# Performance work log

Measured on AMD Instinct MI355X. Metric: run time of the kernel, lower is better.

## Reference

```python
import jax, jax.numpy as jnp
import numpy as np

D_MODEL = 1024
D_FF = 4096
N_HEADS = 16
D_HEAD = D_MODEL // N_HEADS
EPS = 1e-6


def setup_inputs() -> dict:
    key = jax.random.key(0)
    ks = jax.random.split(key, 12)
    B, S = 8, 1024
    s = 1.0 / np.sqrt(D_MODEL)
    inp = {
        "x": jax.random.normal(ks[0], (B, S, D_MODEL), dtype=jnp.float32),
        "mask": jnp.zeros((B, S, S), dtype=bool),
        "gamma1": jnp.ones((D_MODEL,), jnp.float32),
        "beta1": jnp.zeros((D_MODEL,), jnp.float32),
        "Wq": jax.random.normal(ks[1], (D_MODEL, D_MODEL), jnp.float32) * s,
        "bq": jnp.zeros((D_MODEL,), jnp.float32),
        "Wk": jax.random.normal(ks[2], (D_MODEL, D_MODEL), jnp.float32) * s,
        "bk": jnp.zeros((D_MODEL,), jnp.float32),
        "Wv": jax.random.normal(ks[3], (D_MODEL, D_MODEL), jnp.float32) * s,
        "bv": jnp.zeros((D_MODEL,), jnp.float32),
        "Wo": jax.random.normal(ks[4], (D_MODEL, D_MODEL), jnp.float32) * s,
        "bo": jnp.zeros((D_MODEL,), jnp.float32),
        "gamma2": jnp.ones((D_MODEL,), jnp.float32),
        "beta2": jnp.zeros((D_MODEL,), jnp.float32),
        "W1": jax.random.normal(ks[5], (D_MODEL, D_FF), jnp.float32) * s,
        "b1": jnp.zeros((D_FF,), jnp.float32),
        "W2": jax.random.normal(ks[6], (D_FF, D_MODEL), jnp.float32) * (1.0 / np.sqrt(D_FF)),
        "b2": jnp.zeros((D_MODEL,), jnp.float32),
    }
    return inp


def layer_norm(x, gamma, beta):
    mean = jnp.mean(x, axis=-1, keepdims=True)
    var = jnp.mean(jnp.square(x - mean), axis=-1, keepdims=True)  # unbiased=False
    return gamma * (x - mean) / jnp.sqrt(var + EPS) + beta


def mha(x, mask, Wq, bq, Wk, bk, Wv, bv, Wo, bo):
    B, S, _ = x.shape
    # projections: [B,S,D] -> [B,H,S,dh]
    q = (x @ Wq + bq).reshape(B, S, N_HEADS, D_HEAD).transpose(0, 2, 1, 3)
    k = (x @ Wk + bk).reshape(B, S, N_HEADS, D_HEAD).transpose(0, 2, 1, 3)
    v = (x @ Wv + bv).reshape(B, S, N_HEADS, D_HEAD).transpose(0, 2, 1, 3)
    # scores: [B,H,Sq,Sk]
    scores = jnp.einsum("bhqd,bhkd->bhqk", q, k) / np.sqrt(D_HEAD)
    scores = jnp.where(mask[:, None, :, :], -jnp.inf, scores)
    attn = jax.nn.softmax(scores, axis=-1)
    out = jnp.einsum("bhqk,bhkd->bhqd", attn, v)  # [B,H,Sq,dh]
    out = out.transpose(0, 2, 1, 3).reshape(B, S, D_MODEL)
    return out @ Wo + bo


def reference(x, mask, gamma1, beta1, Wq, bq, Wk, bk, Wv, bv, Wo, bo,
              gamma2, beta2, W1, b1, W2, b2):
    # pre-layer-norm variant per source: x = ln1(x); x = x + attn(x); x = ln2(x); x = x + ff(x)
    x = layer_norm(x, gamma1, beta1)
    x = x + mha(x, mask, Wq, bq, Wk, bk, Wv, bv, Wo, bo)
    x = layer_norm(x, gamma2, beta2)
    ff = jax.nn.relu(x @ W1 + b1) @ W2 + b2
    return x + ff
```

## Files before the change

### kernel.cpp

```cpp
#include <hip/hip_runtime.h>
#include <hip/hip_bf16.h>

typedef __bf16 bf16;
typedef __bf16 bf16x8 __attribute__((ext_vector_type(8)));
typedef __bf16 bf16x4 __attribute__((ext_vector_type(4)));
typedef float  f32x4  __attribute__((ext_vector_type(4)));

#define N_HEADS 16
#define D_HEAD  64
#define SEQ     1024
#define BATCH   8
#define MROWS   (BATCH * SEQ)

__device__ __forceinline__ void gld_lds16(const void* g, void* l) {
    __builtin_amdgcn_global_load_lds(
        (const __attribute__((address_space(1))) void*)g,
        (__attribute__((address_space(3))) void*)l, 16, 0, 0);
}

__global__ __launch_bounds__(256)
void wconv_t(const float* __restrict__ W, bf16* __restrict__ Wt, int K, int N)
{
    __shared__ float tile[32][33];
    const int tx = threadIdx.x & 31, ty = threadIdx.x >> 5;
    const int nb = blockIdx.x * 32, kb = blockIdx.y * 32;
    #pragma unroll
    for (int i = 0; i < 4; ++i)
        tile[ty + i * 8][tx] = W[(size_t)(kb + ty + i * 8) * N + nb + tx];
    __syncthreads();
    #pragma unroll
    for (int i = 0; i < 4; ++i)
        Wt[(size_t)(nb + ty + i * 8) * K + kb + tx] = (bf16)tile[tx][ty + i * 8];
}

__global__ __launch_bounds__(256)
void bconcat(const float* __restrict__ bq, const float* __restrict__ bk,
             const float* __restrict__ bv, float* __restrict__ o)
{
    const int i = blockIdx.x * 256 + threadIdx.x;
    if (i < 1024)       o[i] = bq[i];
    else if (i < 2048)  o[i] = bk[i - 1024];
    else if (i < 3072)  o[i] = bv[i - 2048];
}

__global__ __launch_bounds__(256)
void mask_pack(const unsigned char* __restrict__ m,
               unsigned long long* __restrict__ bits)
{
    const int i = blockIdx.x * 256 + threadIdx.x;
    unsigned long long b = __ballot(m[i] != 0);
    if ((threadIdx.x & 63) == 0) bits[i >> 6] = b;
}

__global__ __launch_bounds__(256)
void ln_kernel(const float* __restrict__ x, const float* __restrict__ g,
               const float* __restrict__ b, bf16* __restrict__ obf,
               float* __restrict__ of)
{
    const int row = blockIdx.x;
    const int tid = threadIdx.x;
    const float4 v = ((const float4*)(x + (size_t)row * 1024))[tid];
    float s  = v.x + v.y + v.z + v.w;
    float sq = v.x * v.x + v.y * v.y + v.z * v.z + v.w * v.w;
    #pragma unroll
    for (int off = 32; off; off >>= 1) {
        s  += __shfl_down(s, off);
        sq += __shfl_down(sq, off);
    }
    __shared__ float red[8];
    const int wid = tid >> 6, lid = tid & 63;
    if (lid == 0) { red[wid] = s; red[4 + wid] = sq; }
    __syncthreads();
    if (tid == 0) {
        float ts = red[0] + red[1] + red[2] + red[3];
        float tq = red[4] + red[5] + red[6] + red[7];
        float mean = ts * (1.f / 1024.f);
        float var  = tq * (1.f / 1024.f) - mean * mean;
        red[0] = mean;
        red[1] = rsqrtf(var + 1e-6f);
    }
    __syncthreads();
    const float mean = red[0], rstd = red[1];
    const float4 gg = ((const float4*)g)[tid];
    const float4 bb = ((const float4*)b)[tid];
    float y0 = (v.x - mean) * rstd * gg.x + bb.x;
    float y1 = (v.y - mean) * rstd * gg.y + bb.y;
    float y2 = (v.z - mean) * rstd * gg.z + bb.z;
    float y3 = (v.w - mean) * rstd * gg.w + bb.w;
    float4 o; o.x = y0; o.y = y1; o.z = y2; o.w = y3;
    ((float4*)(of + (size_t)row * 1024))[tid] = o;
    bf16x4 ob; ob[0] = (bf16)y0; ob[1] = (bf16)y1; ob[2] = (bf16)y2; ob[3] = (bf16)y3;
    ((bf16x4*)(obf + (size_t)row * 1024))[tid] = ob;
}

template <int EPI>
__global__ __launch_bounds__(256)
void gemm_bt(const bf16* __restrict__ A, const bf16* __restrict__ Bt,
             const float* __restrict__ bias, const float* __restrict__ resid,
             void* __restrict__ Cout, int M, int N, int K, int nbx)
{
    __shared__ __attribute__((aligned(16))) bf16 a_lds[128 * 64];
    __shared__ __attribute__((aligned(16))) bf16 b_lds[128 * 64];
    const int tid = threadIdx.x;
    const int l = tid & 63, w = tid >> 6;
    const int lo = l & 15, hi = l >> 4;

    const int nwg = gridDim.x;
    const int nid = (blockIdx.x & 7) * (nwg >> 3) + (blockIdx.x >> 3);
    const int bx = nid % nbx, by = nid / nbx;
    const int m0 = by * 128, n0 = bx * 128;

    const int wrow = (w >> 1) * 64, wcol = (w & 1) * 64;
    const int srow = tid >> 3;
    const int c8   = tid & 7;
    const int c8g  = c8 ^ (srow & 7);

    f32x4 acc[4][4];
    #pragma unroll
    for (int i = 0; i < 4; ++i)
        #pragma unroll
        for (int j = 0; j < 4; ++j) acc[i][j] = f32x4{0.f, 0.f, 0.f, 0.f};

    const int nkt = K >> 6;
    for (int kt = 0; kt < nkt; ++kt) {
        __syncthreads();
        const int kc = kt * 64 + c8g * 8;
        #pragma unroll
        for (int blk = 0; blk < 4; ++blk) {
            const int row = blk * 32 + srow;
            gld_lds16(A  + (size_t)(m0 + row) * K + kc, &a_lds[row * 64 + c8 * 8]);
            gld_lds16(Bt + (size_t)(n0 + row) * K + kc, &b_lds[row * 64 + c8 * 8]);
        }
        asm volatile("s_waitcnt vmcnt(0)" ::: "memory");
        __syncthreads();

        #pragma unroll
        for (int kk2 = 0; kk2 < 2; ++kk2) {
            bf16x8 af[4], bfr[4];
            #pragma unroll
            for (int m = 0; m < 4; ++m) {
                const int row = wrow + m * 16 + lo;
                const int ch = ((kk2 * 4 + hi) ^ (lo & 7)) << 3;
                af[m] = *(const bf16x8*)&a_lds[row * 64 + ch];
            }
            #pragma unroll
            for (int n = 0; n < 4; ++n) {
                const int row = wcol + n * 16 + lo;
                const int ch = ((kk2 * 4 + hi) ^ (lo & 7)) << 3;
                bfr[n] = *(const bf16x8*)&b_lds[row * 64 + ch];
            }
            #pragma unroll
            for (int m = 0; m < 4; ++m)
                #pragma unroll
                for (int n = 0; n < 4; ++n)
                    acc[m][n] = __builtin_amdgcn_mfma_f32_16x16x32_bf16(af[m], bfr[n], acc[m][n], 0, 0, 0);
        }
    }

    #pragma unroll
    for (int m = 0; m < 4; ++m) {
        const int Rbase = m0 + wrow + m * 16 + hi * 4;
        #pragma unroll
        for (int n = 0; n < 4; ++n) {
            const int Cc = n0 + wcol + n * 16 + lo;
            const float bv = bias[Cc];
            #pragma unroll
            for (int r = 0; r < 4; ++r) {
                const int Rr = Rbase + r;
                float vv = acc[m][n][r] + bv;
                if (EPI == 0) {
                    const int b_ = Rr >> 10, s_ = Rr & 1023;
                    const int which = Cc >> 10;
                    const int cc = Cc & 1023;
                    const int h_ = cc >> 6, d_ = cc & 63;
                    ((bf16*)Cout)[(size_t)which * ((size_t)MROWS * 1024) +
                                  (((size_t)(b_ * 16 + h_) * 1024 + s_) << 6) + d_] = (bf16)vv;
                } else if (EPI == 1) {
                    vv += resid[(size_t)Rr * N + Cc];
                    ((float*)Cout)[(size_t)Rr * N + Cc] = vv;
                } else {
                    vv = fmaxf(vv, 0.f);
                    ((bf16*)Cout)[(size_t)Rr * N + Cc] = (bf16)vv;
                }
            }
        }
    }
}

__global__ __launch_bounds__(256)
void attn_kernel(const bf16* __restrict__ q, const bf16* __restrict__ k,
                 const bf16* __restrict__ v,
                 const unsigned long long* __restrict__ mbits,
                 bf16* __restrict__ ctx)
{
    __shared__ __attribute__((aligned(16))) bf16 q_lds[64][72];
    __shared__ __attribute__((aligned(16))) bf16 k_lds[64][72];
    __shared__ __attribute__((aligned(16))) bf16 vt_lds[64][72];
    __shared__ __attribute__((aligned(16))) bf16 p_lds[4][16][72];

    const int id = blockIdx.x;
    const int swz = (id & 7) * 256 + (id >> 3);
    const int qt = swz & 15;
    const int bh = swz >> 4;
    const int hh = bh & 15, bb = bh >> 4;
    const int tid = threadIdx.x;
    const int w = tid >> 6, l = tid & 63;
    const int lo = l & 15, hi = l >> 4;

    {
        const bf16* qg = q + ((size_t)bh * SEQ + qt * 64) * D_HEAD;
        #pragma unroll
        for (int i = 0; i < 2; ++i) {
            const int e = (i * 256 + tid) * 8;
            const int r = e >> 6, c = e & 63;
            *(uint4*)&q_lds[r][c] = *(const uint4*)(qg + r * 64 + c);
        }
    }

    f32x4 oacc[4];
    float m_r[4], l_r[4];
    #pragma unroll
    for (int i = 0; i < 4; ++i) {
        oacc[i] = f32x4{0.f, 0.f, 0.f, 0.f};
        m_r[i] = -__builtin_inff();
        l_r[i] = 0.f;
    }

    for (int kt = 0; kt < 16; ++kt) {
        __syncthreads();
        const bf16* kg = k + ((size_t)bh * SEQ + kt * 64) * D_HEAD;
        const bf16* vg = v + ((size_t)bh * SEQ + kt * 64) * D_HEAD;
        #pragma unroll
        for (int i = 0; i < 2; ++i) {
            const int e = (i * 256 + tid) * 8;
            const int r = e >> 6, c = e & 63;
            *(uint4*)&k_lds[r][c] = *(const uint4*)(kg + r * 64 + c);
            uint4 tv = *(const uint4*)(vg + r * 64 + c);
            const bf16* pv = (const bf16*)&tv;
            const int colS = r ^ (((c >> 3) & 7) << 3);
            #pragma unroll
            for (int j = 0; j < 8; ++j) vt_lds[c + j][colS] = pv[j];
        }
        unsigned long long mb[4];
        #pragma unroll
        for (int r = 0; r < 4; ++r) {
            const int qrow = qt * 64 + w * 16 + hi * 4 + r;
            mb[r] = mbits[((((size_t)bb << 10) | qrow) << 4) + kt];
        }
        __syncthreads();

        f32x4 sf[4];
        #pragma unroll
        for (int ct = 0; ct < 4; ++ct) {
            f32x4 sa = f32x4{0.f, 0.f, 0.f, 0.f};
            #pragma unroll
            for (int kk = 0; kk < 2; ++kk) {
                bf16x8 a   = *(const bf16x8*)&q_lds[w * 16 + lo][kk * 32 + hi * 8];
                bf16x8 bfr = *(const bf16x8*)&k_lds[ct * 16 + lo][kk * 32 + hi * 8];
                sa = __builtin_amdgcn_mfma_f32_16x16x32_bf16(a, bfr, sa, 0, 0, 0);
            }
            sf[ct] = sa;
        }

        float pm[4];
        #pragma unroll
        for (int r = 0; r < 4; ++r) {
            #pragma unroll
            for (int ct = 0; ct < 4; ++ct) {
                float sv = sf[ct][r] * 0.125f;
                if ((mb[r] >> (ct * 16 + lo)) & 1ull) sv = -__builtin_inff();
                sf[ct][r] = sv;
            }
            float t0 = fmaxf(fmaxf(sf[0][r], sf[1][r]), fmaxf(sf[2][r], sf[3][r]));
            #pragma unroll
            for (int off = 1; off < 16; off <<= 1) t0 = fmaxf(t0, __shfl_xor(t0, off));
            pm[r] = t0;
        }
        float scl[4];
        #pragma unroll
        for (int r = 0; r < 4; ++r) {
            const float mn = fmaxf(m_r[r], pm[r]);
            scl[r] = __expf(m_r[r] - mn);
            m_r[r] = mn;
            float acc_s = 0.f;
            #pragma unroll
            for (int ct = 0; ct < 4; ++ct) {
                const float p = __expf(sf[ct][r] - mn);
                sf[ct][r] = p;
                acc_s += p;
            }
            #pragma unroll
            for (int off = 1; off < 16; off <<= 1) acc_s += __shfl_xor(acc_s, off);
            l_r[r] = l_r[r] * scl[r] + acc_s;
        }
        #pragma unroll
        for (int n = 0; n < 4; ++n)
            #pragma unroll
            for (int r = 0; r < 4; ++r) oacc[n][r] *= scl[r];

        #pragma unroll
        for (int ct = 0; ct < 4; ++ct)
            #pragma unroll
            for (int r = 0; r < 4; ++r)
                p_lds[w][hi * 4 + r][ct * 16 + lo] = (bf16)sf[ct][r];
        asm volatile("s_waitcnt lgkmcnt(0)" ::: "memory");

        #pragma unroll
        for (int n = 0; n < 4; ++n) {
            const int g = (((n * 16 + lo) >> 3) & 7) << 3;
            #pragma unroll
            for (int kk = 0; kk < 2; ++kk) {
                bf16x8 a   = *(const bf16x8*)&p_lds[w][lo][kk * 32 + hi * 8];
                bf16x8 bfr = *(const bf16x8*)&vt_lds[n * 16 + lo][(kk * 32 + hi * 8) ^ g];
                oacc[n] = __builtin_amdgcn_mfma_f32_16x16x32_bf16(a, bfr, oacc[n], 0, 0, 0);
            }
        }
    }

    #pragma unroll
    for (int r = 0; r < 4; ++r) {
        const float inv = 1.f / l_r[r];
        const size_t srow = (size_t)bb * SEQ + qt * 64 + w * 16 + hi * 4 + r;
        const size_t base = (srow * N_HEADS + hh) * D_HEAD;
        #pragma unroll
        for (int n = 0; n < 4; ++n)
            ctx[base + n * 16 + lo] = (bf16)(oacc[n][r] * inv);
    }
}

extern "C" void kernel_launch(void* const* d_in, const int* in_sizes, int n_in,
                              void* d_out, int out_size, void* d_ws, size_t ws_size,
                              hipStream_t stream)
{
    const float* x      = (const float*)d_in[0];
    const unsigned char* mask = (const unsigned char*)d_in[1];
    const float* gamma1 = (const float*)d_in[2];
    const float* beta1  = (const float*)d_in[3];
    const float* Wq     = (const float*)d_in[4];
    const float* bq     = (const float*)d_in[5];
    const float* Wk     = (const float*)d_in[6];
    const float* bk     = (const float*)d_in[7];
    const float* Wv     = (const float*)d_in[8];
    const float* bv     = (const float*)d_in[9];
    const float* Wo     = (const float*)d_in[10];
    const float* bo     = (const float*)d_in[11];
    const float* gamma2 = (const float*)d_in[12];
    const float* beta2  = (const float*)d_in[13];
    const float* W1     = (const float*)d_in[14];
    const float* b1     = (const float*)d_in[15];
    const float* W2     = (const float*)d_in[16];
    const float* b2     = (const float*)d_in[17];

    char* ws = (char*)d_ws;
    const size_t MB = 1u << 20;
    bf16* wqkv = (bf16*)(ws + 0 * MB);
    bf16* wot  = (bf16*)(ws + 6 * MB);
    bf16* w1t  = (bf16*)(ws + 8 * MB);
    bf16* w2t  = (bf16*)(ws + 16 * MB);
    unsigned long long* mbits = (unsigned long long*)(ws + 16 * MB);
    float* bqkv = (float*)(ws + 17 * MB);
    bf16* xn1b = (bf16*)(ws + 24 * MB);
    float* xn1f = (float*)(ws + 40 * MB);
    bf16* qkv  = (bf16*)(ws + 72 * MB);
    bf16* ctx  = (bf16*)(ws + 120 * MB);
    bf16* hbuf = (bf16*)(ws + 72 * MB);
    bf16* xn2b = (bf16*)(ws + 136 * MB);
    float* xn2f = (float*)(ws + 152 * MB);
    float* x2f = (float*)d_out;

    wconv_t<<<dim3(32, 32),  256, 0, stream>>>(Wq, wqkv,               1024, 1024);
    wconv_t<<<dim3(32, 32),  256, 0, stream>>>(Wk, wqkv + 1024 * 1024, 1024, 1024);
    wconv_t<<<dim3(32, 32),  256, 0, stream>>>(Wv, wqkv + 2048 * 1024, 1024, 1024);
    wconv_t<<<dim3(32, 32),  256, 0, stream>>>(Wo, wot, 1024, 1024);
    wconv_t<<<dim3(128, 32), 256, 0, stream>>>(W1, w1t, 1024, 4096);
    bconcat<<<12, 256, 0, stream>>>(bq, bk, bv, bqkv);
    mask_pack<<<32768, 256, 0, stream>>>(mask, mbits);

    ln_kernel<<<MROWS, 256, 0, stream>>>(x, gamma1, beta1, xn1b, xn1f);

    gemm_bt<0><<<24 * 64, 256, 0, stream>>>(xn1b, wqkv, bqkv, nullptr, qkv, MROWS, 3072, 1024, 24);

    attn_kernel<<<2048, 256, 0, stream>>>(qkv, qkv + (size_t)MROWS * 1024,
                                          qkv + (size_t)2 * MROWS * 1024, mbits, ctx);

    wconv_t<<<dim3(32, 128), 256, 0, stream>>>(W2, w2t, 4096, 1024);

    gemm_bt<1><<<8 * 64, 256, 0, stream>>>(ctx, wot, bo, xn1f, x2f, MROWS, 1024, 1024, 8);

    ln_kernel<<<MROWS, 256, 0, stream>>>(x2f, gamma2, beta2, xn2b, xn2f);

    gemm_bt<2><<<32 * 64, 256, 0, stream>>>(xn2b, w1t, b1, nullptr, hbuf, MROWS, 4096, 1024, 32);

    gemm_bt<1><<<8 * 64, 256, 0, stream>>>(hbuf, w2t, b2, xn2f, (float*)d_out, MROWS, 1024, 4096, 8);
}
```

Measured before the change: 634.1 us.

## Double-buffer K/V in attention, compute transposed scores, lazy rescale softmax

```diff
diff --git a/kernel.cpp b/kernel.cpp
--- a/kernel.cpp
+++ b/kernel.cpp
@@ -193,10 +193,9 @@
                  const unsigned long long* __restrict__ mbits,
                  bf16* __restrict__ ctx)
 {
-    __shared__ __attribute__((aligned(16))) bf16 q_lds[64][72];
-    __shared__ __attribute__((aligned(16))) bf16 k_lds[64][72];
-    __shared__ __attribute__((aligned(16))) bf16 vt_lds[64][72];
-    __shared__ __attribute__((aligned(16))) bf16 p_lds[4][16][72];
+    __shared__ __attribute__((aligned(16))) bf16 k_lds[2][64][72];
+    __shared__ __attribute__((aligned(16))) bf16 vt_lds[2][64][72];
+    __shared__ __attribute__((aligned(16))) bf16 qp_lds[64][72];
 
     const int id = blockIdx.x;
     const int swz = (id & 7) * 256 + (id >> 3);
@@ -207,102 +206,121 @@
     const int w = tid >> 6, l = tid & 63;
     const int lo = l & 15, hi = l >> 4;
 
-    {
-        const bf16* qg = q + ((size_t)bh * SEQ + qt * 64) * D_HEAD;
-        #pragma unroll
-        for (int i = 0; i < 2; ++i) {
-            const int e = (i * 256 + tid) * 8;
-            const int r = e >> 6, c = e & 63;
-            *(uint4*)&q_lds[r][c] = *(const uint4*)(qg + r * 64 + c);
-        }
+    const bf16* qg = q + ((size_t)bh * SEQ + qt * 64) * D_HEAD;
+    const bf16* kg = k + (size_t)bh * SEQ * D_HEAD;
+    const bf16* vg = v + (size_t)bh * SEQ * D_HEAD;
+
+    uint4 kreg[2], vreg[2];
+    #pragma unroll
+    for (int i = 0; i < 2; ++i) {
+        const int e = (i * 256 + tid) * 8;
+        const int r = e >> 6, c = e & 63;
+        *(uint4*)&qp_lds[r][c] = *(const uint4*)(qg + r * 64 + c);
+        kreg[i] = *(const uint4*)(kg + r * 64 + c);
+        vreg[i] = *(const uint4*)(vg + r * 64 + c);
+    }
+    __syncthreads();
+
+    bf16x8 qf[2];
+    #pragma unroll
+    for (int kk = 0; kk < 2; ++kk)
+        qf[kk] = *(const bf16x8*)&qp_lds[w * 16 + lo][kk * 32 + hi * 8];
+
+    #pragma unroll
+    for (int i = 0; i < 2; ++i) {
+        const int e = (i * 256 + tid) * 8;
+        const int r = e >> 6, c = e & 63;
+        *(uint4*)&k_lds[0][r][c] = kreg[i];
+        const bf16* pv = (const bf16*)&vreg[i];
+        const int colS = r ^ (((c >> 3) & 7) << 3);
+        #pragma unroll
+        for (int j = 0; j < 8; ++j) vt_lds[0][c + j][colS] = pv[j];
     }
 
     f32x4 oacc[4];
-    float m_r[4], l_r[4];
-    #pragma unroll
-    for (int i = 0; i < 4; ++i) {
-        oacc[i] = f32x4{0.f, 0.f, 0.f, 0.f};
-        m_r[i] = -__builtin_inff();
-        l_r[i] = 0.f;
-    }
+    #pragma unroll
+    for (int i = 0; i < 4; ++i) oacc[i] = f32x4{0.f, 0.f, 0.f, 0.f};
+    float m_q = -__builtin_inff(), l_q = 0.f;
+
+    const int qrow = qt * 64 + w * 16 + lo;
+    const size_t mbase = (((size_t)bb << 10) | (size_t)qrow) << 4;
+
+    __syncthreads();
 
     for (int kt = 0; kt < 16; ++kt) {
-        __syncthreads();
-        const bf16* kg = k + ((size_t)bh * SEQ + kt * 64) * D_HEAD;
-        const bf16* vg = v + ((size_t)bh * SEQ + kt * 64) * D_HEAD;
-        #pragma unroll
-        for (int i = 0; i < 2; ++i) {
-            const int e = (i * 256 + tid) * 8;
-            const int r = e >> 6, c = e & 63;
-            *(uint4*)&k_lds[r][c] = *(const uint4*)(kg + r * 64 + c);
-            uint4 tv = *(const uint4*)(vg + r * 64 + c);
-            const bf16* pv = (const bf16*)&tv;
-            const int colS = r ^ (((c >> 3) & 7) << 3);
-            #pragma unroll
-            for (int j = 0; j < 8; ++j) vt_lds[c + j][colS] = pv[j];
-        }
-        unsigned long long mb[4];
-        #pragma unroll
-        for (int r = 0; r < 4; ++r) {
-            const int qrow = qt * 64 + w * 16 + hi * 4 + r;
-            mb[r] = mbits[((((size_t)bb << 10) | qrow) << 4) + kt];
-        }
-        __syncthreads();
-
-        f32x4 sf[4];
+        const int cur = kt & 1, nxt = cur ^ 1;
+        if (kt < 15) {
+            const bf16* kgn = kg + (size_t)(kt + 1) * 64 * D_HEAD;
+            const bf16* vgn = vg + (size_t)(kt + 1) * 64 * D_HEAD;
+            #pragma unroll
+            for (int i = 0; i < 2; ++i) {
+                const int e = (i * 256 + tid) * 8;
+                const int r = e >> 6, c = e & 63;
+                kreg[i] = *(const uint4*)(kgn + r * 64 + c);
+                vreg[i] = *(const uint4*)(vgn + r * 64 + c);
+            }
+        }
+        const unsigned long long mb = mbits[mbase + kt];
+
+        f32x4 st[4];
         #pragma unroll
         for (int ct = 0; ct < 4; ++ct) {
             f32x4 sa = f32x4{0.f, 0.f, 0.f, 0.f};
             #pragma unroll
             for (int kk = 0; kk < 2; ++kk) {
-                bf16x8 a   = *(const bf16x8*)&q_lds[w * 16 + lo][kk * 32 + hi * 8];
-                bf16x8 bfr = *(const bf16x8*)&k_lds[ct * 16 + lo][kk * 32 + hi * 8];
-                sa = __builtin_amdgcn_mfma_f32_16x16x32_bf16(a, bfr, sa, 0, 0, 0);
-            }
-            sf[ct] = sa;
-        }
-
-        float pm[4];
-        #pragma unroll
-        for (int r = 0; r < 4; ++r) {
-            #pragma unroll
-            for (int ct = 0; ct < 4; ++ct) {
-                float sv = sf[ct][r] * 0.125f;
-                if ((mb[r] >> (ct * 16 + lo)) & 1ull) sv = -__builtin_inff();
-                sf[ct][r] = sv;
-            }
-            float t0 = fmaxf(fmaxf(sf[0][r], sf[1][r]), fmaxf(sf[2][r], sf[3][r]));
-            #pragma unroll
-            for (int off = 1; off < 16; off <<= 1) t0 = fmaxf(t0, __shfl_xor(t0, off));
-            pm[r] = t0;
-        }
-        float scl[4];
-        #pragma unroll
-        for (int r = 0; r < 4; ++r) {
-            const float mn = fmaxf(m_r[r], pm[r]);
-            scl[r] = __expf(m_r[r] - mn);
-            m_r[r] = mn;
-            float acc_s = 0.f;
-            #pragma unroll
-            for (int ct = 0; ct < 4; ++ct) {
-                const float p = __expf(sf[ct][r] - mn);
-                sf[ct][r] = p;
-                acc_s += p;
-            }
-            #pragma unroll
-            for (int off = 1; off < 16; off <<= 1) acc_s += __shfl_xor(acc_s, off);
-            l_r[r] = l_r[r] * scl[r] + acc_s;
-        }
-        #pragma unroll
-        for (int n = 0; n < 4; ++n)
-            #pragma unroll
-            for (int r = 0; r < 4; ++r) oacc[n][r] *= scl[r];
+                bf16x8 kf = *(const bf16x8*)&k_lds[cur][ct * 16 + lo][kk * 32 + hi * 8];
+                sa = __builtin_amdgcn_mfma_f32_16x16x32_bf16(kf, qf[kk], sa, 0, 0, 0);
+            }
+            st[ct] = sa;
+        }
 
         #pragma unroll
         for (int ct = 0; ct < 4; ++ct)
             #pragma unroll
+            for (int r = 0; r < 4; ++r) {
+                float sv = st[ct][r] * 0.125f;
+                if ((mb >> (ct * 16 + hi * 4 + r)) & 1ull) sv = -__builtin_inff();
+                st[ct][r] = sv;
+            }
+
+        float tmax = st[0][0];
+        #pragma unroll
+        for (int ct = 0; ct < 4; ++ct)
+            #pragma unroll
             for (int r = 0; r < 4; ++r)
-                p_lds[w][hi * 4 + r][ct * 16 + lo] = (bf16)sf[ct][r];
+                if (ct + r) tmax = fmaxf(tmax, st[ct][r]);
+        tmax = fmaxf(tmax, __shfl_xor(tmax, 16));
+        tmax = fmaxf(tmax, __shfl_xor(tmax, 32));
+
+        if (!__all(tmax - m_q <= 8.f)) {
+            const float nm = fmaxf(m_q, tmax);
+            const float scl = __expf(m_q - nm);
+            m_q = nm;
+            l_q *= scl;
+            #pragma unroll
+            for (int r = 0; r < 4; ++r) {
+                const float so = __shfl(scl, hi * 4 + r);
+                #pragma unroll
+                for (int n = 0; n < 4; ++n) oacc[n][r] *= so;
+            }
+        }
+
+        float ps = 0.f;
+        #pragma unroll
+        for (int ct = 0; ct < 4; ++ct) {
+            bf16x4 pv4;
+            #pragma unroll
+            for (int r = 0; r < 4; ++r) {
+                const float p = __expf(st[ct][r] - m_q);
+                ps += p;
+                pv4[r] = (bf16)p;
+            }
+            *(bf16x4*)&qp_lds[w * 16 + lo][ct * 16 + hi * 4] = pv4;
+        }
+        ps += __shfl_xor(ps, 16);
+        ps += __shfl_xor(ps, 32);
+        l_q += ps;
+
         asm volatile("s_waitcnt lgkmcnt(0)" ::: "memory");
 
         #pragma unroll
@@ -310,16 +328,31 @@
             const int g = (((n * 16 + lo) >> 3) & 7) << 3;
             #pragma unroll
             for (int kk = 0; kk < 2; ++kk) {
-                bf16x8 a   = *(const bf16x8*)&p_lds[w][lo][kk * 32 + hi * 8];
-                bf16x8 bfr = *(const bf16x8*)&vt_lds[n * 16 + lo][(kk * 32 + hi * 8) ^ g];
-                oacc[n] = __builtin_amdgcn_mfma_f32_16x16x32_bf16(a, bfr, oacc[n], 0, 0, 0);
-            }
-        }
+                bf16x8 a  = *(const bf16x8*)&qp_lds[w * 16 + lo][kk * 32 + hi * 8];
+                bf16x8 bv = *(const bf16x8*)&vt_lds[cur][n * 16 + lo][(kk * 32 + hi * 8) ^ g];
+                oacc[n] = __builtin_amdgcn_mfma_f32_16x16x32_bf16(a, bv, oacc[n], 0, 0, 0);
+            }
+        }
+
+        if (kt < 15) {
+            #pragma unroll
+            for (int i = 0; i < 2; ++i) {
+                const int e = (i * 256 + tid) * 8;
+                const int r = e >> 6, c = e & 63;
+                *(uint4*)&k_lds[nxt][r][c] = kreg[i];
+                const bf16* pv = (const bf16*)&vreg[i];
+                const int colS = r ^ (((c >> 3) & 7) << 3);
+                #pragma unroll
+                for (int j = 0; j < 8; ++j) vt_lds[nxt][c + j][colS] = pv[j];
+            }
+        }
+        __syncthreads();
     }
 
     #pragma unroll
     for (int r = 0; r < 4; ++r) {
-        const float inv = 1.f / l_r[r];
+        const float lr = __shfl(l_q, hi * 4 + r);
+        const float inv = 1.f / lr;
         const size_t srow = (size_t)bb * SEQ + qt * 64 + w * 16 + hi * 4 + r;
         const size_t base = (srow * N_HEADS + hh) * D_HEAD;
         #pragma unroll
```

Result: no change. 623.6 us (-1.6%).
